# Kernel tuning notes

Hardware: AMD Instinct MI355X
Metric: run time of the kernel (lower is better)

The kernel has to match this reference:

```python
import jax, jax.numpy as jnp
import numpy as np

N_USERS = 100_000
N_ITEMS = 50_000
N = N_USERS + N_ITEMS
E = 1_000_000
D = 64          # emb_size
H = 4           # head_num
DH = D // H
L_GT = 2
L_GCN = 2


def setup_inputs() -> dict:
    key = jax.random.key(0)
    ks = jax.random.split(key, 8)
    rows = jax.random.randint(ks[0], (E,), 0, N, dtype=jnp.int32)
    cols = jax.random.randint(ks[1], (E,), 0, N, dtype=jnp.int32)
    vals = jax.random.uniform(ks[2], (E,), dtype=jnp.float32)
    user_emb = jax.random.normal(ks[3], (N_USERS, D), dtype=jnp.float32) * 0.1
    item_emb = jax.random.normal(ks[4], (N_ITEMS, D), dtype=jnp.float32) * 0.1
    scale = 1.0 / np.sqrt(D)  # ~xavier
    Wq = jax.random.normal(ks[5], (L_GT, D, D), dtype=jnp.float32) * scale
    Wk = jax.random.normal(ks[6], (L_GT, D, D), dtype=jnp.float32) * scale
    Wv = jax.random.normal(ks[7], (L_GT, D, D), dtype=jnp.float32) * scale
    return {"rows": rows, "cols": cols, "vals": vals,
            "user_emb": user_emb, "item_emb": item_emb,
            "Wq": Wq, "Wk": Wk, "Wv": Wv}


def _spmm(rows, cols, vals, embeds):
    # torch.spmm(adj, embeds) with adj in COO form -> segment-sum over edges
    return jax.ops.segment_sum(vals[:, None] * embeds[cols], rows, num_segments=N)


def _gt_layer(rows, cols, embeds, wq, wk, wv):
    rowE = embeds[rows]                                   # [E, D] gather
    colE = embeds[cols]                                   # [E, D] gather
    q = (rowE @ wq).reshape(E, H, DH)
    k = (colE @ wk).reshape(E, H, DH)
    v = (colE @ wv).reshape(E, H, DH)
    att = jnp.clip(jnp.einsum('ehd,ehd->eh', q, k), -10.0, 10.0)
    expAtt = jnp.exp(att)                                 # [E, H]
    attNorm = jax.ops.segment_sum(expAtt, rows, num_segments=N)[rows]  # scatter-softmax denom
    att = expAtt / (attNorm + 1e-8)
    res = (att[..., None] * v).reshape(E, D)
    return jax.ops.segment_sum(res, rows, num_segments=N)  # [N, D]


def reference(rows, cols, vals, user_emb, item_emb, Wq, Wk, Wv):
    embeds = jnp.concatenate([user_emb, item_emb], axis=0)  # [N, D]
    embeds_lst = [embeds]
    for l in range(L_GT):
        embeds_lst.append(_gt_layer(rows, cols, embeds_lst[-1], Wq[l], Wk[l], Wv[l]))
    for _ in range(L_GCN):
        embeds_lst.append(_spmm(rows, cols, vals, embeds_lst[-1]))
    out = embeds_lst[0]
    for e in embeds_lst[1:]:
        out = out + e
    return out
```

## Files before the change

kernel.cpp:

```cpp
#include <hip/hip_runtime.h>

#define NUSERS 100000
#define NITEMS 50000
#define NTOT   150000
#define NEDGE  1000000
#define NTILE  9375

typedef unsigned int uint32;
typedef __attribute__((ext_vector_type(8))) short short8;
typedef __attribute__((ext_vector_type(4))) float f32x4;

__device__ __forceinline__ unsigned short f2bf(float f) {
  unsigned int u = __float_as_uint(f);
  u += 0x7FFFu + ((u >> 16) & 1u);
  return (unsigned short)(u >> 16);
}
__device__ __forceinline__ uint32 pack2bf(float a, float b) {
  return (uint32)f2bf(a) | ((uint32)f2bf(b) << 16);
}
__device__ __forceinline__ float bf_lo(uint32 u) { return __uint_as_float(u << 16); }
__device__ __forceinline__ float bf_hi(uint32 u) { return __uint_as_float(u & 0xFFFF0000u); }

__global__ void k_init(const float* __restrict__ ue, const float* __restrict__ ie,
                       uint32* __restrict__ embb) {
  int i = blockIdx.x * 256 + threadIdx.x;
  if (i >= NTOT * 16) return;
  float4 v = (i < NUSERS * 16) ? ((const float4*)ue)[i]
                               : ((const float4*)ie)[i - NUSERS * 16];
  uint2 pk;
  pk.x = pack2bf(v.x, v.y);
  pk.y = pack2bf(v.z, v.w);
  ((uint2*)embb)[i] = pk;
}

__global__ void k_wpack(const float* __restrict__ Wq, const float* __restrict__ Wk,
                        const float* __restrict__ Wv, uint32* __restrict__ Wbg) {
  int t = blockIdx.x * 256 + threadIdx.x;
  if (t >= 12288) return;
  int l = t / 6144, rem = t % 6144, mat = rem / 2048, j = rem % 2048;
  int n = j >> 5, k2 = j & 31;
  const float* W = (mat == 0 ? Wq : mat == 1 ? Wk : Wv) + l * 4096;
  Wbg[t] = pack2bf(W[k2 * 128 + n], W[k2 * 128 + 64 + n]);
}

__global__ void k_hist(const int* __restrict__ rows, int* __restrict__ cnt) {
  int e = blockIdx.x * 256 + threadIdx.x;
  if (e < NEDGE) atomicAdd(&cnt[rows[e]], 1);
}

__global__ void k_scan1(const int* __restrict__ cnt, int* __restrict__ partial,
                        int* __restrict__ blocksums) {
  __shared__ int s[256];
  int t = threadIdx.x, b = blockIdx.x;
  int base = b * 2048 + t * 8;
  int pre[8]; int sum = 0;
  #pragma unroll
  for (int j = 0; j < 8; ++j) {
    int idx = base + j;
    int x = (idx < NTOT) ? cnt[idx] : 0;
    pre[j] = sum; sum += x;
  }
  s[t] = sum; __syncthreads();
  for (int off = 1; off < 256; off <<= 1) {
    int x = (t >= off) ? s[t - off] : 0;
    __syncthreads(); s[t] += x; __syncthreads();
  }
  int excl = s[t] - sum;
  #pragma unroll
  for (int j = 0; j < 8; ++j) {
    int idx = base + j;
    if (idx < NTOT) partial[idx] = excl + pre[j];
  }
  if (t == 255) blocksums[b] = s[255];
}

__global__ void k_scan2(const int* __restrict__ blocksums, int* __restrict__ blockoffs, int nblk) {
  __shared__ int s[128];
  int t = threadIdx.x;
  int x = (t < nblk) ? blocksums[t] : 0;
  s[t] = x; __syncthreads();
  for (int off = 1; off < 128; off <<= 1) {
    int y = (t >= off) ? s[t - off] : 0;
    __syncthreads(); s[t] += y; __syncthreads();
  }
  if (t < nblk) blockoffs[t] = s[t] - x;
}

__global__ void k_scan3(int* __restrict__ row_ptr, const int* __restrict__ blockoffs,
                        int* __restrict__ cursor) {
  int i = blockIdx.x * 256 + threadIdx.x;
  if (i < NTOT) {
    int v = row_ptr[i] + blockoffs[i >> 11];
    row_ptr[i] = v; cursor[i] = v;
  }
  if (i == 0) row_ptr[NTOT] = NEDGE;
}

__global__ void k_fill(const int* __restrict__ rows, const int* __restrict__ cols,
                       const float* __restrict__ vals, int* __restrict__ cursor,
                       int* __restrict__ ecols, float* __restrict__ evals) {
  int e = blockIdx.x * 256 + threadIdx.x;
  if (e >= NEDGE) return;
  int r = rows[e];
  int pos = atomicAdd(&cursor[r], 1);
  ecols[pos] = cols[e];
  evals[pos] = vals[e];
}

__global__ void __launch_bounds__(256) k_qkv(const uint32* __restrict__ embb,
    const uint32* __restrict__ Wbg, float* __restrict__ Q, uint32* __restrict__ KVb) {
  __shared__ float scr[4][2][16][68];
  int t = threadIdx.x;
  int wave = t >> 6, lane = t & 63;
  int tile = blockIdx.x * 4 + wave;
  if (tile >= NTILE) return;
  int c = lane & 15, quad = lane >> 4;
  int nodeBase = tile * 16;
  const uint32* arow = embb + (nodeBase + c) * 32 + quad * 4;
  uint4 a0u = *(const uint4*)arow;
  uint4 a1u = *(const uint4*)(arow + 16);
  short8 a0 = *(short8*)&a0u;
  short8 a1 = *(short8*)&a1u;
  float (*SK)[68] = scr[wave][0];
  float (*SV)[68] = scr[wave][1];
  const uint32* wbase = Wbg + c * 32 + quad * 4;
  #pragma unroll
  for (int mat = 0; mat < 3; ++mat) {
    f32x4 acc[4];
    #pragma unroll
    for (int nt = 0; nt < 4; ++nt) acc[nt] = (f32x4){0.f, 0.f, 0.f, 0.f};
    const uint32* wb = wbase + mat * 2048;
    #pragma unroll
    for (int nt = 0; nt < 4; ++nt) {
      uint4 b0u = *(const uint4*)(wb + nt * 512);
      uint4 b1u = *(const uint4*)(wb + nt * 512 + 16);
      short8 b0 = *(short8*)&b0u;
      short8 b1 = *(short8*)&b1u;
      acc[nt] = __builtin_amdgcn_mfma_f32_16x16x32_bf16(a0, b0, acc[nt], 0, 0, 0);
      acc[nt] = __builtin_amdgcn_mfma_f32_16x16x32_bf16(a1, b1, acc[nt], 0, 0, 0);
    }
    float (*S)[68] = (mat == 2) ? SV : SK;
    #pragma unroll
    for (int nt = 0; nt < 4; ++nt)
      #pragma unroll
      for (int r = 0; r < 4; ++r)
        S[quad * 4 + r][nt * 16 + c] = acc[nt][r];
    if (mat == 0) {
      #pragma unroll
      for (int i = 0; i < 4; ++i) {
        int node = i * 4 + quad;
        f32x4 q4 = *(f32x4*)&SK[node][c * 4];
        *(f32x4*)&Q[(nodeBase + node) * 64 + c * 4] = q4;
      }
    } else if (mat == 2) {
      #pragma unroll
      for (int i = 0; i < 4; ++i) {
        int node = i * 4 + quad;
        f32x4 K4 = *(f32x4*)&SK[node][c * 4];
        f32x4 V4 = *(f32x4*)&SV[node][c * 4];
        uint4 o;
        o.x = pack2bf(K4[0], K4[1]);
        o.y = pack2bf(K4[2], K4[3]);
        o.z = pack2bf(V4[0], V4[1]);
        o.w = pack2bf(V4[2], V4[3]);
        *(uint4*)&KVb[(nodeBase + node) * 64 + c * 4] = o;
      }
    }
  }
}

__global__ void __launch_bounds__(256) k_gt(const float* __restrict__ Q,
    const uint32* __restrict__ KVb, const int* __restrict__ row_ptr,
    const int* __restrict__ ecols, float* __restrict__ emb_out,
    uint32* __restrict__ embb_out) {
  int t = threadIdx.x;
  int n = blockIdx.x * 4 + (t >> 6);
  if (n >= NTOT) return;
  int lane = t & 63;
  int es = lane >> 4;
  int dl = lane & 15;
  float4 q4 = *(const float4*)&Q[n * 64 + dl * 4];
  int s     = __builtin_amdgcn_readfirstlane(row_ptr[n]);
  int e_end = __builtin_amdgcn_readfirstlane(row_ptr[n + 1]);
  int cnt = e_end - s;
  int li = s + lane;
  int cv = ecols[li < NEDGE ? li : NEDGE - 1];
  float den = 0.f;
  float4 acc = make_float4(0.f, 0.f, 0.f, 0.f);
  #pragma unroll 2
  for (int base = 0; base < cnt; base += 4) {
    int i = base + es;
    int cc;
    if (base < 64) cc = __shfl(cv, i & 63);
    else           cc = (i < cnt) ? ecols[s + i] : 0;
    float ex = 0.f;
    float4 v4 = make_float4(0.f, 0.f, 0.f, 0.f);
    if (i < cnt) {
      uint4 w = *(const uint4*)&KVb[cc * 64 + dl * 4];
      float kx = bf_lo(w.x), ky = bf_hi(w.x);
      float kz = bf_lo(w.y), kw = bf_hi(w.y);
      v4.x = bf_lo(w.z); v4.y = bf_hi(w.z);
      v4.z = bf_lo(w.w); v4.w = bf_hi(w.w);
      float x = q4.x * kx + q4.y * ky + q4.z * kz + q4.w * kw;
      x += __shfl_xor(x, 1);
      x += __shfl_xor(x, 2);
      x = fminf(fmaxf(x, -10.f), 10.f);
      ex = __expf(x);
    }
    den += ex;
    acc.x = fmaf(ex, v4.x, acc.x);
    acc.y = fmaf(ex, v4.y, acc.y);
    acc.z = fmaf(ex, v4.z, acc.z);
    acc.w = fmaf(ex, v4.w, acc.w);
  }
  #pragma unroll
  for (int off = 16; off <= 32; off <<= 1) {
    den  += __shfl_xor(den, off);
    acc.x += __shfl_xor(acc.x, off);
    acc.y += __shfl_xor(acc.y, off);
    acc.z += __shfl_xor(acc.z, off);
    acc.w += __shfl_xor(acc.w, off);
  }
  float inv = 1.f / (den + 1e-8f);
  float4 r = make_float4(acc.x * inv, acc.y * inv, acc.z * inv, acc.w * inv);
  if (es == 0) {
    *(float4*)&emb_out[n * 64 + dl * 4] = r;
  } else if (es == 1) {
    uint2 pk;
    pk.x = pack2bf(r.x, r.y);
    pk.y = pack2bf(r.z, r.w);
    *(uint2*)&embb_out[n * 32 + dl * 2] = pk;
  }
}

template<int FINAL>
__global__ void __launch_bounds__(256) k_gcn(const float* __restrict__ emb,
    const int* __restrict__ row_ptr, const int* __restrict__ ecols,
    const float* __restrict__ evals, float* __restrict__ emb_out,
    const float* __restrict__ ue, const float* __restrict__ ie,
    const float* __restrict__ add1, const float* __restrict__ add2) {
  int t = threadIdx.x;
  int n = blockIdx.x * 4 + (t >> 6);
  if (n >= NTOT) return;
  int lane = t & 63;
  int s     = __builtin_amdgcn_readfirstlane(row_ptr[n]);
  int e_end = __builtin_amdgcn_readfirstlane(row_ptr[n + 1]);
  float a[8];
  #pragma unroll
  for (int j = 0; j < 8; ++j) a[j] = 0.f;
  for (int p = s; p < e_end; p += 8) {
    #pragma unroll
    for (int j = 0; j < 8; ++j) {
      int pj = p + j;
      int pc = (pj < e_end) ? pj : s;
      float w = (pj < e_end) ? evals[pc] : 0.f;
      int c = ecols[pc];
      a[j] = fmaf(w, emb[c * 64 + lane], a[j]);
    }
  }
  float acc = ((a[0] + a[1]) + (a[2] + a[3])) + ((a[4] + a[5]) + (a[6] + a[7]));
  int base = n * 64 + lane;
  if (FINAL) {
    float b = (n < NUSERS) ? ue[base] : ie[base - NUSERS * 64];
    acc += b + add1[base] + add2[base] + emb[base];
  }
  emb_out[base] = acc;
}

extern "C" void kernel_launch(void* const* d_in, const int* in_sizes, int n_in,
                              void* d_out, int out_size, void* d_ws, size_t ws_size,
                              hipStream_t stream) {
  const int*   rows = (const int*)d_in[0];
  const int*   cols = (const int*)d_in[1];
  const float* vals = (const float*)d_in[2];
  const float* ue   = (const float*)d_in[3];
  const float* ie   = (const float*)d_in[4];
  const float* Wq   = (const float*)d_in[5];
  const float* Wk   = (const float*)d_in[6];
  const float* Wv   = (const float*)d_in[7];
  float* out = (float*)d_out;

  char* p = (char*)d_ws;
  auto alloc = [&](size_t b) { char* r = p; p += (b + 255) & ~(size_t)255; return (void*)r; };
  int*   cnt     = (int*)alloc((size_t)NTOT * 4);
  int*   row_ptr = (int*)alloc((size_t)(NTOT + 1) * 4);
  int*   cursor  = (int*)alloc((size_t)NTOT * 4);
  int*   bsums   = (int*)alloc(128 * 4);
  int*   boffs   = (int*)alloc(128 * 4);
  int*   ecols   = (int*)alloc((size_t)NEDGE * 4);
  float* evals   = (float*)alloc((size_t)NEDGE * 4);
  uint32* Wbg  = (uint32*)alloc((size_t)12288 * 4);
  float*  Q    = (float*)alloc((size_t)NTOT * 64 * 4);
  uint32* KVb  = (uint32*)alloc((size_t)NTOT * 64 * 4);
  float*  embA = (float*)alloc((size_t)NTOT * 64 * 4);
  float*  embB = (float*)alloc((size_t)NTOT * 64 * 4);
  uint32* embb0 = (uint32*)alloc((size_t)NTOT * 32 * 4);
  uint32* embb1 = (uint32*)alloc((size_t)NTOT * 32 * 4);

  hipMemsetAsync(cnt, 0, (size_t)NTOT * 4, stream);
  k_hist<<<(NEDGE + 255) / 256, 256, 0, stream>>>(rows, cnt);
  int nblk = (NTOT + 2047) / 2048;
  k_scan1<<<nblk, 256, 0, stream>>>(cnt, row_ptr, bsums);
  k_scan2<<<1, 128, 0, stream>>>(bsums, boffs, nblk);
  k_scan3<<<(NTOT + 255) / 256, 256, 0, stream>>>(row_ptr, boffs, cursor);
  k_fill<<<(NEDGE + 255) / 256, 256, 0, stream>>>(rows, cols, vals, cursor, ecols, evals);
  k_wpack<<<48, 256, 0, stream>>>(Wq, Wk, Wv, Wbg);
  k_init<<<(NTOT * 16 + 255) / 256, 256, 0, stream>>>(ue, ie, embb0);

  k_qkv<<<(NTILE + 3) / 4, 256, 0, stream>>>(embb0, Wbg, Q, KVb);
  k_gt<<<(NTOT + 3) / 4, 256, 0, stream>>>(Q, KVb, row_ptr, ecols, embA, embb1);
  k_qkv<<<(NTILE + 3) / 4, 256, 0, stream>>>(embb1, Wbg + 6144, Q, KVb);
  k_gt<<<(NTOT + 3) / 4, 256, 0, stream>>>(Q, KVb, row_ptr, ecols, embB, embb0);
  k_gcn<0><<<(NTOT + 3) / 4, 256, 0, stream>>>(embB, row_ptr, ecols, evals, Q,
                                               nullptr, nullptr, nullptr, nullptr);
  k_gcn<1><<<(NTOT + 3) / 4, 256, 0, stream>>>(Q, row_ptr, ecols, evals, out,
                                               ue, ie, embA, embB);
}
```

Baseline: 524.1 us.

## Gather bf16 embeddings in GCN layers with half-wave edge split and shuffled indices

The GCN propagation kernels now gather neighbour rows from packed bf16 copies instead of fp32, halving gather bytes per edge. Each wave splits into two halves that process alternate edges, and the first 64 edge indices and weights are loaded once and broadcast by shuffle. The first GCN layer also writes a bf16 copy for the second layer, and the final add is split across both halves. This cuts memory traffic in the gather-bound SpMM at the cost of bf16 rounding in the GCN inputs.

```diff
diff --git a/kernel.cpp b/kernel.cpp
--- a/kernel.cpp
+++ b/kernel.cpp
@@ -234,37 +234,64 @@
 }
 
 template<int FINAL>
-__global__ void __launch_bounds__(256) k_gcn(const float* __restrict__ emb,
+__global__ void __launch_bounds__(256) k_gcn(const uint32* __restrict__ src,
     const int* __restrict__ row_ptr, const int* __restrict__ ecols,
     const float* __restrict__ evals, float* __restrict__ emb_out,
+    uint32* __restrict__ embb_out,
     const float* __restrict__ ue, const float* __restrict__ ie,
-    const float* __restrict__ add1, const float* __restrict__ add2) {
+    const float* __restrict__ add1, const float* __restrict__ add2,
+    const float* __restrict__ addG) {
   int t = threadIdx.x;
   int n = blockIdx.x * 4 + (t >> 6);
   if (n >= NTOT) return;
   int lane = t & 63;
+  int eh = lane >> 5;
+  int dl = lane & 31;
   int s     = __builtin_amdgcn_readfirstlane(row_ptr[n]);
   int e_end = __builtin_amdgcn_readfirstlane(row_ptr[n + 1]);
-  float a[8];
-  #pragma unroll
-  for (int j = 0; j < 8; ++j) a[j] = 0.f;
-  for (int p = s; p < e_end; p += 8) {
+  int cnt = e_end - s;
+  int li = s + lane;
+  int pli = li < NEDGE ? li : NEDGE - 1;
+  int   cv = ecols[pli];
+  float wv = evals[pli];
+  float ax[8], ay[8];
+  #pragma unroll
+  for (int j = 0; j < 8; ++j) { ax[j] = 0.f; ay[j] = 0.f; }
+  for (int p = 0; p < cnt; p += 16) {
     #pragma unroll
     for (int j = 0; j < 8; ++j) {
-      int pj = p + j;
-      int pc = (pj < e_end) ? pj : s;
-      float w = (pj < e_end) ? evals[pc] : 0.f;
-      int c = ecols[pc];
-      a[j] = fmaf(w, emb[c * 64 + lane], a[j]);
+      int i = p + 2 * j + eh;
+      bool ok = i < cnt;
+      int ii = ok ? i : 0;
+      int cc; float w;
+      if (ii < 64) { cc = __shfl(cv, ii); w = __shfl(wv, ii); }
+      else         { cc = ecols[s + ii];  w = evals[s + ii]; }
+      if (!ok) w = 0.f;
+      uint32 g = src[cc * 32 + dl];
+      ax[j] = fmaf(w, bf_lo(g), ax[j]);
+      ay[j] = fmaf(w, bf_hi(g), ay[j]);
     }
   }
-  float acc = ((a[0] + a[1]) + (a[2] + a[3])) + ((a[4] + a[5]) + (a[6] + a[7]));
-  int base = n * 64 + lane;
+  float sx = ((ax[0] + ax[1]) + (ax[2] + ax[3])) + ((ax[4] + ax[5]) + (ax[6] + ax[7]));
+  float sy = ((ay[0] + ay[1]) + (ay[2] + ay[3])) + ((ay[4] + ay[5]) + (ay[6] + ay[7]));
+  sx += __shfl_xor(sx, 32);
+  sy += __shfl_xor(sy, 32);
   if (FINAL) {
-    float b = (n < NUSERS) ? ue[base] : ie[base - NUSERS * 64];
-    acc += b + add1[base] + add2[base] + emb[base];
-  }
-  emb_out[base] = acc;
+    const float* p1 = (eh == 0)
+        ? ((n < NUSERS) ? ue + (size_t)n * 64 : ie + (size_t)(n - NUSERS) * 64)
+        : add2 + (size_t)n * 64;
+    const float* p2 = (eh == 0) ? add1 + (size_t)n * 64 : addG + (size_t)n * 64;
+    float2 u = *(const float2*)&p1[dl * 2];
+    float2 v = *(const float2*)&p2[dl * 2];
+    float px = u.x + v.x, py = u.y + v.y;
+    px += __shfl_xor(px, 32);
+    py += __shfl_xor(py, 32);
+    sx += px; sy += py;
+    if (eh == 0) *(float2*)&emb_out[(size_t)n * 64 + dl * 2] = make_float2(sx, sy);
+  } else {
+    if (eh == 0) *(float2*)&emb_out[(size_t)n * 64 + dl * 2] = make_float2(sx, sy);
+    else         embb_out[n * 32 + dl] = pack2bf(sx, sy);
+  }
 }
 
 extern "C" void kernel_launch(void* const* d_in, const int* in_sizes, int n_in,
@@ -311,8 +338,8 @@
   k_gt<<<(NTOT + 3) / 4, 256, 0, stream>>>(Q, KVb, row_ptr, ecols, embA, embb1);
   k_qkv<<<(NTILE + 3) / 4, 256, 0, stream>>>(embb1, Wbg + 6144, Q, KVb);
   k_gt<<<(NTOT + 3) / 4, 256, 0, stream>>>(Q, KVb, row_ptr, ecols, embB, embb0);
-  k_gcn<0><<<(NTOT + 3) / 4, 256, 0, stream>>>(embB, row_ptr, ecols, evals, Q,
-                                               nullptr, nullptr, nullptr, nullptr);
-  k_gcn<1><<<(NTOT + 3) / 4, 256, 0, stream>>>(Q, row_ptr, ecols, evals, out,
-                                               ue, ie, embA, embB);
-}
+  k_gcn<0><<<(NTOT + 3) / 4, 256, 0, stream>>>(embb0, row_ptr, ecols, evals, Q, embb1,
+                                               nullptr, nullptr, nullptr, nullptr, nullptr);
+  k_gcn<1><<<(NTOT + 3) / 4, 256, 0, stream>>>(embb1, row_ptr, ecols, evals, out, nullptr,
+                                               ue, ie, embA, embB, Q);
+}
```

After: 572.5 us. 9.2% more time.
